# Kernel optimization log

Measured on AMD Instinct MI355X. Metric: run time of the kernel, lower is better.

The kernel has to match this reference:

```python
import jax, jax.numpy as jnp
import numpy as np

N, E = 384, 3072          # nodes, relation pairs
CIN, EMB, D = 4096, 200, 512  # roi feat dim, glove dim, hidden dim
NOBJ, NREL = 151, 51
NUM_ITER = 3
ALPHA = 0.5


def setup_inputs() -> dict:
    key = jax.random.key(0)
    ks = iter(jax.random.split(key, 64))

    def w(shape, scale=0.02):
        return jax.random.normal(next(ks), shape, dtype=jnp.float32) * scale

    inp = {
        'x': jax.random.normal(next(ks), (N, CIN), dtype=jnp.float32),
        'pos_info': jax.random.uniform(next(ks), (N, 9), dtype=jnp.float32),
        'union_features': jax.random.normal(next(ks), (E, CIN), dtype=jnp.float32),
        'obj_labels': jax.random.randint(next(ks), (N,), 0, NOBJ, dtype=jnp.int32),
        'rel_pair_idx': jax.random.randint(next(ks), (E, 2), 0, N, dtype=jnp.int32),
        # embeddings
        'obj_embed1_w': w((NOBJ, EMB)),
        'obj_embed2_w': w((NOBJ, EMB)),
        # node/edge embeddings
        'node_emb_w': w((D, CIN + EMB + 128)), 'node_emb_b': jnp.zeros((D,)),
        'node_emb2_w': w((D, CIN + EMB + D)), 'node_emb2_b': jnp.zeros((D,)),
        'edge_emb_w': w((D, CIN)), 'edge_emb_b': jnp.zeros((D,)),
        # pos_embed: Linear(9,32) -> BN(32) -> Linear(32,128) -> ReLU
        'pos_w1': w((32, 9)), 'pos_b1': jnp.zeros((32,)),
        'pos_gamma': jnp.ones((32,)), 'pos_beta': jnp.zeros((32,)),
        'pos_w2': w((128, 32)), 'pos_b2': jnp.zeros((128,)),
        # node GRUCell (with bias), edge GRUCell (no bias); gate order r,z,n
        'ngate_wih': w((3 * D, D)), 'ngate_whh': w((3 * D, D)),
        'ngate_bih': jnp.zeros((3 * D,)), 'ngate_bhh': jnp.zeros((3 * D,)),
        'egate_wih': w((3 * D, D)), 'egate_whh': w((3 * D, D)),
        # message kernels
        'n2n_w1': w((D, D)), 'n2n_b1': jnp.zeros((D,)),
        'n2n_w2': w((D, D)), 'n2n_b2': jnp.zeros((D,)),
        'e2n_w1': w((D, D)), 'e2n_b1': jnp.zeros((D,)),
        'e2n_w2': w((D, D)), 'e2n_b2': jnp.zeros((D,)),
        # node2edge 1x1 convs == pointwise linears
        'n2e_w1': w((D, 2 * D)), 'n2e_b1': jnp.zeros((D,)),
        'n2e_w2': w((D, D)), 'n2e_b2': jnp.zeros((D,)),
        'rel_cls_w': w((NREL, D)), 'rel_cls_b': jnp.zeros((NREL,)),
    }
    return inp


def _gru(x, h, wih, whh, bih=None, bhh=None):
    gi = x @ wih.T
    gh = h @ whh.T
    if bih is not None:
        gi = gi + bih
        gh = gh + bhh
    ir, iz, ig = jnp.split(gi, 3, axis=-1)
    hr, hz, hg = jnp.split(gh, 3, axis=-1)
    r = jax.nn.sigmoid(ir + hr)
    z = jax.nn.sigmoid(iz + hz)
    g = jnp.tanh(ig + r * hg)
    return (1.0 - z) * g + z * h


def _mlp2(h, w1, b1, w2, b2):
    h = jax.nn.relu(h @ w1.T + b1)
    return jax.nn.relu(h @ w2.T + b2)


def reference(x, pos_info, union_features, obj_labels, rel_pair_idx,
              obj_embed1_w, obj_embed2_w,
              node_emb_w, node_emb_b, node_emb2_w, node_emb2_b,
              edge_emb_w, edge_emb_b,
              pos_w1, pos_b1, pos_gamma, pos_beta, pos_w2, pos_b2,
              ngate_wih, ngate_whh, ngate_bih, ngate_bhh,
              egate_wih, egate_whh,
              n2n_w1, n2n_b1, n2n_w2, n2n_b2,
              e2n_w1, e2n_b1, e2n_w2, e2n_b2,
              n2e_w1, n2e_b1, n2e_w2, n2e_b2,
              rel_cls_w, rel_cls_b):
    n = x.shape[0]
    # pos embed (BatchNorm in training mode = batch stats)
    ph = pos_info @ pos_w1.T + pos_b1
    mu, var = ph.mean(0), ph.var(0)
    ph = (ph - mu) * jax.lax.rsqrt(var + 1e-5) * pos_gamma + pos_beta
    pos_embed = jax.nn.relu(ph @ pos_w2.T + pos_b2)

    obj_embed = obj_embed1_w[obj_labels]  # predcls: GT labels
    node_states = jnp.concatenate([x, obj_embed, pos_embed], -1) @ node_emb_w.T + node_emb_b

    p0, p1 = rel_pair_idx[:, 0], rel_pair_idx[:, 1]
    adj = jnp.zeros((n, n), jnp.float32).at[p0, p1].set(1.0)
    edge_rep = union_features @ edge_emb_w.T + edge_emb_b
    # torch sparse to_dense sums duplicate indices
    edge_states = jnp.zeros((n, n, D), jnp.float32).at[p0, p1].add(edge_rep)

    deg = adj.sum(1, keepdims=True) + 1e-6
    for _ in range(NUM_ITER):
        n2n = (adj @ node_states) / deg
        e2n = jnp.einsum('ij,ijd->jd', adj, edge_states)
        n2n = _mlp2(n2n, n2n_w1, n2n_b1, n2n_w2, n2n_b2)
        e2n = _mlp2(e2n, e2n_w1, e2n_b1, e2n_w2, e2n_b2)
        node_states = _gru(ALPHA * n2n + (1.0 - ALPHA) * e2n, node_states,
                           ngate_wih, ngate_whh, ngate_bih, ngate_bhh)

    # predcls: obj_dists = to_onehot(labels), preds = labels
    obj_dists = jnp.full((n, NOBJ), -1000.0, jnp.float32).at[jnp.arange(n), obj_labels].set(1000.0)
    node_states = jnp.concatenate([x, node_states, obj_embed2_w[obj_labels]], -1) @ node_emb2_w.T + node_emb2_b

    for _ in range(NUM_ITER):
        # all-pairs direction-aware concat, masked by adjacency
        ek = jnp.concatenate([
            jnp.broadcast_to(node_states[:, None, :], (n, n, D)),
            jnp.broadcast_to(node_states[None, :, :], (n, n, D)),
        ], -1) * adj[:, :, None]                      # [n, n, 2D]
        msg = _mlp2(ek, n2e_w1, n2e_b1, n2e_w2, n2e_b2)  # 1x1 convs == pointwise
        edge_states = _gru(msg.reshape(n * n, D), edge_states.reshape(n * n, D),
                           egate_wih, egate_whh).reshape(n, n, D)

    rel_feats = edge_states[p0, p1]
    rel_dists = rel_feats @ rel_cls_w.T + rel_cls_b
    return obj_dists, rel_dists
```

## Files before the change

### kernel.cpp

```cpp
#include <hip/hip_runtime.h>

typedef unsigned short ushort_t;
typedef unsigned int uint_t;

#define N_    384
#define E_    3072
#define CIN_  4096
#define EMB_  200
#define D_    512
#define NOBJ_ 151
#define NREL_ 51
#define K1_   (CIN_ + EMB_ + 128)
#define K1P_  4448
#define K2_   (CIN_ + EMB_ + D_)
#define K2P_  4832

__device__ __forceinline__ ushort_t f2b(float f) {
    uint_t u = __float_as_uint(f);
    u += 0x7FFFu + ((u >> 16) & 1u);
    return (ushort_t)(u >> 16);
}

__global__ void k_pair_min(const int* __restrict__ rp, int* __restrict__ mapMin) {
    int e = blockIdx.x * blockDim.x + threadIdx.x;
    if (e >= E_) return;
    atomicMin(&mapMin[rp[2 * e] * N_ + rp[2 * e + 1]], e);
}
__global__ void k_pair_rep(const int* __restrict__ rp, const int* __restrict__ mapMin,
                           int* __restrict__ rep, int* __restrict__ deg_cnt) {
    int e = blockIdx.x * blockDim.x + threadIdx.x;
    if (e >= E_) return;
    int r = mapMin[rp[2 * e] * N_ + rp[2 * e + 1]];
    rep[e] = r;
    if (r == e) atomicAdd(&deg_cnt[rp[2 * e]], 1);
}
__global__ void k_inv_deg(const int* __restrict__ deg_cnt, float* __restrict__ inv_deg) {
    int i = blockIdx.x * blockDim.x + threadIdx.x;
    if (i < N_) inv_deg[i] = 1.0f / ((float)deg_cnt[i] + 1e-6f);
}

__global__ __launch_bounds__(1024) void k_pos_a(const float* __restrict__ pi,
                                                const float* __restrict__ w1,
                                                const float* __restrict__ b1,
                                                const float* __restrict__ g,
                                                const float* __restrict__ be,
                                                float* __restrict__ posn) {
    __shared__ float ph[N_ * 32];
    __shared__ float mu_s[32], rs_s[32];
    int tid = threadIdx.x;
    for (int idx = tid; idx < N_ * 32; idx += 1024) {
        int i = idx >> 5, f = idx & 31;
        float s = b1[f];
        for (int k = 0; k < 9; ++k) s += pi[i * 9 + k] * w1[f * 9 + k];
        ph[idx] = s;
    }
    __syncthreads();
    if (tid < 32) {
        float s = 0.f;
        for (int i = 0; i < N_; ++i) s += ph[i * 32 + tid];
        float m = s / N_;
        float v = 0.f;
        for (int i = 0; i < N_; ++i) { float d = ph[i * 32 + tid] - m; v += d * d; }
        mu_s[tid] = m;
        rs_s[tid] = rsqrtf(v / N_ + 1e-5f);
    }
    __syncthreads();
    for (int idx = tid; idx < N_ * 32; idx += 1024) {
        int f = idx & 31;
        posn[idx] = (ph[idx] - mu_s[f]) * rs_s[f] * g[f] + be[f];
    }
}
__global__ void k_pos2(const float* __restrict__ pn, const float* __restrict__ w,
                       const float* __restrict__ b, float* __restrict__ out) {
    int idx = blockIdx.x * blockDim.x + threadIdx.x;
    if (idx >= N_ * 128) return;
    int i = idx / 128, f = idx % 128;
    float s = b[f];
    for (int k = 0; k < 32; ++k) s += pn[i * 32 + k] * w[f * 32 + k];
    out[idx] = fmaxf(s, 0.f);
}

__global__ void k_build_A1b(const float* __restrict__ x, const int* __restrict__ lab,
                            const float* __restrict__ emb1, const float* __restrict__ pe,
                            ushort_t* __restrict__ A) {
    int idx = blockIdx.x * blockDim.x + threadIdx.x;
    if (idx >= N_ * K1P_) return;
    int i = idx / K1P_, c = idx % K1P_;
    float v = 0.f;
    if (c < CIN_)             v = x[(size_t)i * CIN_ + c];
    else if (c < CIN_ + EMB_) v = emb1[lab[i] * EMB_ + (c - CIN_)];
    else if (c < K1_)         v = pe[i * 128 + (c - CIN_ - EMB_)];
    A[idx] = f2b(v);
}
__global__ void k_build_A2b(const float* __restrict__ x, const int* __restrict__ lab,
                            const float* __restrict__ emb2, const ushort_t* __restrict__ nsb,
                            ushort_t* __restrict__ A) {
    int idx = blockIdx.x * blockDim.x + threadIdx.x;
    if (idx >= N_ * K2P_) return;
    int i = idx / K2P_, c = idx % K2P_;
    ushort_t o = 0;
    if (c < CIN_)             o = f2b(x[(size_t)i * CIN_ + c]);
    else if (c < CIN_ + D_)   o = nsb[i * D_ + (c - CIN_)];
    else if (c < K2_)         o = f2b(emb2[lab[i] * EMB_ + (c - CIN_ - D_)]);
    A[idx] = o;
}
__global__ void k_build_ekb(const int* __restrict__ rp, const ushort_t* __restrict__ nsb,
                            ushort_t* __restrict__ ek) {
    int idx = blockIdx.x * blockDim.x + threadIdx.x;
    if (idx >= E_ * 2 * D_) return;
    int e = idx / (2 * D_), c = idx % (2 * D_);
    ek[idx] = (c < D_) ? nsb[rp[2 * e] * D_ + c] : nsb[rp[2 * e + 1] * D_ + (c - D_)];
}

struct ConvDesc { const float* src; ushort_t* dst; int K, Kp, rows, rowsp; };
struct ConvArgs { ConvDesc d[16]; };
__global__ void k_conv_batch(ConvArgs a) {
    ConvDesc c = a.d[blockIdx.y];
    for (int row = blockIdx.x; row < c.rowsp; row += gridDim.x) {
        const float* src = c.src + (size_t)row * c.K;
        ushort_t* dst = c.dst + (size_t)row * c.Kp;
        bool inrow = row < c.rows;
        for (int k = threadIdx.x * 4; k < c.Kp; k += blockDim.x * 4) {
            uint2 ov = {0u, 0u};
            if (inrow && k < c.K) {
                float4 v = *(const float4*)(src + k);
                ov.x = (uint_t)f2b(v.x) | ((uint_t)f2b(v.y) << 16);
                ov.y = (uint_t)f2b(v.z) | ((uint_t)f2b(v.w) << 16);
            }
            *(uint2*)(dst + k) = ov;
        }
    }
}
__global__ void k_f2b_n(const float* __restrict__ s, ushort_t* __restrict__ d, int n) {
    int i = blockIdx.x * blockDim.x + threadIdx.x;
    if (i < n) d[i] = f2b(s[i]);
}

__global__ void k_scatter_edge(const float* __restrict__ er, const int* __restrict__ rep,
                               float* __restrict__ es) {
    int e = blockIdx.x;
    int d = blockIdx.y * 256 + threadIdx.x;
    atomicAdd(&es[(size_t)rep[e] * D_ + d], er[(size_t)e * D_ + d]);
}
__global__ void k_broadcast_es(const int* __restrict__ rep, float* __restrict__ es,
                               ushort_t* __restrict__ esb) {
    int idx = blockIdx.x * blockDim.x + threadIdx.x;
    if (idx >= E_ * D_) return;
    int e = idx / D_, d = idx % D_;
    float v = es[(size_t)rep[e] * D_ + d];
    es[idx] = v;
    esb[idx] = f2b(v);
}
__global__ void k_scatter_e2n(const int* __restrict__ rp, const int* __restrict__ rep,
                              const float* __restrict__ es, float* __restrict__ e2n) {
    int e = blockIdx.x;
    if (rep[e] != e) return;
    int d = blockIdx.y * 256 + threadIdx.x;
    atomicAdd(&e2n[rp[2 * e + 1] * D_ + d], es[(size_t)e * D_ + d]);
}
__global__ void k_scatter_n2n(const int* __restrict__ rp, const int* __restrict__ rep,
                              const float* __restrict__ ns, float* __restrict__ n2n) {
    int e = blockIdx.x;
    if (rep[e] != e) return;
    int d = blockIdx.y * 256 + threadIdx.x;
    atomicAdd(&n2n[rp[2 * e] * D_ + d], ns[rp[2 * e + 1] * D_ + d]);
}
__global__ void k_scale_rows_b(const float* __restrict__ a, const float* __restrict__ inv_deg,
                               ushort_t* __restrict__ ob) {
    int idx = blockIdx.x * blockDim.x + threadIdx.x;
    if (idx >= N_ * D_) return;
    ob[idx] = f2b(a[idx] * inv_deg[idx / D_]);
}
__global__ void k_combine_b(const float* __restrict__ araw, const float* __restrict__ b2,
                            const float* __restrict__ e2nm, ushort_t* __restrict__ o) {
    int idx = blockIdx.x * blockDim.x + threadIdx.x;
    if (idx >= N_ * D_) return;
    float a = fmaxf(araw[idx] + b2[idx & (D_ - 1)], 0.f);
    o[idx] = f2b(0.5f * a + 0.5f * e2nm[idx]);
}
__global__ void k_epi(const float* __restrict__ raw, const float* __restrict__ bias,
                      float* __restrict__ fo, ushort_t* __restrict__ bo,
                      int total, int colmask, int relu) {
    int idx = blockIdx.x * blockDim.x + threadIdx.x;
    if (idx >= total) return;
    float v = raw[idx] + bias[idx & colmask];
    if (relu) v = fmaxf(v, 0.f);
    if (fo) fo[idx] = v;
    if (bo) bo[idx] = f2b(v);
}
__global__ void k_epi_rel(const float* __restrict__ raw, const float* __restrict__ relb,
                          float* __restrict__ out) {
    int idx = blockIdx.x * blockDim.x + threadIdx.x;
    if (idx >= E_ * NREL_) return;
    int row = idx / NREL_, col = idx % NREL_;
    out[idx] = raw[row * 64 + col] + relb[col];
}
__global__ void k_gru(const float* __restrict__ gi, const float* __restrict__ gh,
                      const float* __restrict__ bih, const float* __restrict__ bhh,
                      float* __restrict__ h, ushort_t* __restrict__ hb, int M) {
    int idx = blockIdx.x * blockDim.x + threadIdx.x;
    if (idx >= M * D_) return;
    int m = idx / D_, d = idx % D_;
    size_t b3 = (size_t)m * 3 * D_;
    float ir = gi[b3 + d], iz = gi[b3 + D_ + d], ig = gi[b3 + 2 * D_ + d];
    float hr = gh[b3 + d], hz = gh[b3 + D_ + d], hg = gh[b3 + 2 * D_ + d];
    if (bih) { ir += bih[d]; iz += bih[D_ + d]; ig += bih[2 * D_ + d]; }
    if (bhh) { hr += bhh[d]; hz += bhh[D_ + d]; hg += bhh[2 * D_ + d]; }
    float r = 1.f / (1.f + expf(-(ir + hr)));
    float z = 1.f / (1.f + expf(-(iz + hz)));
    float g = tanhf(ig + r * hg);
    size_t hi = (size_t)m * D_ + d;
    float nv = (1.f - z) * g + z * h[hi];
    h[hi] = nv;
    if (hb) hb[hi] = f2b(nv);
}
__global__ void k_obj_dists(const int* __restrict__ lab, float* __restrict__ out) {
    int idx = blockIdx.x * blockDim.x + threadIdx.x;
    if (idx >= N_ * NOBJ_) return;
    out[idx] = (idx % NOBJ_ == lab[idx / NOBJ_]) ? 1000.f : -1000.f;
}

typedef __attribute__((ext_vector_type(8))) short sh8;
typedef __attribute__((ext_vector_type(4))) float f32x4;

#define GLOAD_LDS16(gp, lp)                                                        \
    __builtin_amdgcn_global_load_lds((__attribute__((address_space(1))) void*)(gp),\
                                     (__attribute__((address_space(3))) void*)(lp),\
                                     16, 0, 0)

template <bool SWZ>
__device__ __forceinline__ void get_bxyz(int& bx, int& by, int& bz) {
    if (!SWZ) { bx = blockIdx.x; by = blockIdx.y; bz = blockIdx.z; return; }
    int nx = gridDim.x, nz = gridDim.z;
    int bid = blockIdx.x + nx * (blockIdx.y + gridDim.y * blockIdx.z);
    int r8 = bid & 7, i = bid >> 3;
    int per = nx * nz;
    int ygrp = i / per;
    int rem = i - ygrp * per;
    bx = rem % nx;
    bz = rem / nx;
    by = r8 + 8 * ygrp;
}

template <int FM, int FN>
__device__ __forceinline__ void gemm_kloop(ushort_t* As, ushort_t* Bs,
                                           const ushort_t* __restrict__ A,
                                           const ushort_t* __restrict__ B,
                                           f32x4 (&acc)[FM][FN],
                                           int K, int ks0, int ks1, int bm, int bn) {
    constexpr int BM = FM * 32, BN = FN * 32;
    constexpr int ATILES = (BM + 63) / 64, BTILES = (BN + 63) / 64;
    const int tid = threadIdx.x;
    const int lane = tid & 63, wid = tid >> 6;
    const int wr = wid >> 1, wc = wid & 1;
    const int ar = tid >> 2, ac = (tid & 3) * 8;
    const int l15 = lane & 15, lg = lane >> 4;
    for (int ks = ks0; ks < ks1; ++ks) {
        int k0 = ks * 32;
#pragma unroll
        for (int i = 0; i < ATILES; ++i) {
            int r = i * 64 + ar;
            if ((BM & 63) == 0 || r < BM)
                GLOAD_LDS16(A + (size_t)(bm + r) * K + k0 + ac, &As[r * 32 + ac]);
        }
#pragma unroll
        for (int i = 0; i < BTILES; ++i) {
            int r = i * 64 + ar;
            if ((BN & 63) == 0 || r < BN)
                GLOAD_LDS16(B + (size_t)(bn + r) * K + k0 + ac, &Bs[r * 32 + ac]);
        }
        __syncthreads();
        sh8 af[FM], bf[FN];
#pragma unroll
        for (int m = 0; m < FM; ++m)
            af[m] = *(const sh8*)&As[(wr * FM * 16 + m * 16 + l15) * 32 + lg * 8];
#pragma unroll
        for (int n = 0; n < FN; ++n)
            bf[n] = *(const sh8*)&Bs[(wc * FN * 16 + n * 16 + l15) * 32 + lg * 8];
#pragma unroll
        for (int m = 0; m < FM; ++m)
#pragma unroll
            for (int n = 0; n < FN; ++n)
                acc[m][n] = __builtin_amdgcn_mfma_f32_16x16x32_bf16(af[m], bf[n], acc[m][n], 0, 0, 0);
        __syncthreads();
    }
}

template <int FM, int FN, bool SWZ = false>
__global__ __launch_bounds__(256) void gemm_mfma(const ushort_t* __restrict__ A,
                                                 const ushort_t* __restrict__ B,
                                                 const float* __restrict__ bias,
                                                 float* __restrict__ C,
                                                 ushort_t* __restrict__ Cb,
                                                 int M, int N, int K, int relu) {
    __shared__ ushort_t As[FM * 32 * 32];
    __shared__ ushort_t Bs[FN * 32 * 32];
    int bx, by, bz;
    get_bxyz<SWZ>(bx, by, bz);
    const int bm = by * FM * 32, bn = bx * FN * 32;
    f32x4 acc[FM][FN];
#pragma unroll
    for (int m = 0; m < FM; ++m)
#pragma unroll
        for (int n = 0; n < FN; ++n) acc[m][n] = (f32x4){0.f, 0.f, 0.f, 0.f};
    gemm_kloop<FM, FN>(As, Bs, A, B, acc, K, 0, K / 32, bm, bn);
    const int lane = threadIdx.x & 63, wid = threadIdx.x >> 6;
    const int l15 = lane & 15, lg = lane >> 4;
    const int r0 = bm + (wid >> 1) * FM * 16, c0 = bn + (wid & 1) * FN * 16;
#pragma unroll
    for (int m = 0; m < FM; ++m)
#pragma unroll
        for (int n = 0; n < FN; ++n)
#pragma unroll
            for (int j = 0; j < 4; ++j) {
                int row = r0 + m * 16 + lg * 4 + j;
                int col = c0 + n * 16 + l15;
                if (row < M && col < N) {
                    float v = acc[m][n][j] + (bias ? bias[col] : 0.f);
                    if (relu) v = fmaxf(v, 0.f);
                    if (C)  C[(size_t)row * N + col] = v;
                    if (Cb) Cb[(size_t)row * N + col] = f2b(v);
                }
            }
}

template <int FM, int FN, bool SWZ = false>
__global__ __launch_bounds__(256) void gemm_splitk(const ushort_t* __restrict__ A,
                                                   const ushort_t* __restrict__ B,
                                                   float* __restrict__ C,
                                                   int M, int N, int K, int S) {
    __shared__ ushort_t As[FM * 32 * 32];
    __shared__ ushort_t Bs[FN * 32 * 32];
    int bx, by, bz;
    get_bxyz<SWZ>(bx, by, bz);
    const int nsteps = K / 32;
    const int ss = (nsteps + S - 1) / S;
    const int ks0 = bz * ss;
    const int ks1 = min(nsteps, ks0 + ss);
    if (ks0 >= ks1) return;
    const int bm = by * FM * 32, bn = bx * FN * 32;
    f32x4 acc[FM][FN];
#pragma unroll
    for (int m = 0; m < FM; ++m)
#pragma unroll
        for (int n = 0; n < FN; ++n) acc[m][n] = (f32x4){0.f, 0.f, 0.f, 0.f};
    gemm_kloop<FM, FN>(As, Bs, A, B, acc, K, ks0, ks1, bm, bn);
    const int lane = threadIdx.x & 63, wid = threadIdx.x >> 6;
    const int l15 = lane & 15, lg = lane >> 4;
    const int r0 = bm + (wid >> 1) * FM * 16, c0 = bn + (wid & 1) * FN * 16;
#pragma unroll
    for (int m = 0; m < FM; ++m)
#pragma unroll
        for (int n = 0; n < FN; ++n)
#pragma unroll
            for (int j = 0; j < 4; ++j) {
                int row = r0 + m * 16 + lg * 4 + j;
                int col = c0 + n * 16 + l15;
                if (row < M && col < N)
                    atomicAdd(&C[(size_t)row * N + col], acc[m][n][j]);
            }
}

__global__ __launch_bounds__(256) void k_ghe_gru(const ushort_t* __restrict__ esb_in,
                                                 const ushort_t* __restrict__ W,
                                                 const float* __restrict__ gi,
                                                 const float* __restrict__ es_in,
                                                 float* __restrict__ es_out,
                                                 ushort_t* __restrict__ esb_out) {
    __shared__ ushort_t As[64 * 32];
    __shared__ ushort_t Bs[96 * 32];
    int bid = blockIdx.x + gridDim.x * blockIdx.y;
    int r8 = bid & 7, i = bid >> 3;
    int per = gridDim.x;
    int ygrp = i / per;
    int x = i - ygrp * per;
    int y = r8 + 8 * ygrp;
    const int bm = y * 64;
    const int dcol0 = x * 32;
    const int tid = threadIdx.x;
    const int lane = tid & 63, wid = tid >> 6;
    const int wr = wid >> 1, wc = wid & 1;
    const int ar = tid >> 2, ac = (tid & 3) * 8;
    const int l15 = lane & 15, lg = lane >> 4;
    f32x4 acc[2][3];
#pragma unroll
    for (int m = 0; m < 2; ++m)
#pragma unroll
        for (int g = 0; g < 3; ++g) acc[m][g] = (f32x4){0.f, 0.f, 0.f, 0.f};

    for (int k0 = 0; k0 < D_; k0 += 32) {
        GLOAD_LDS16(esb_in + (size_t)(bm + ar) * D_ + k0 + ac, &As[ar * 32 + ac]);
        {
            int rr = ar;
            int wrow = (rr >> 5) * D_ + dcol0 + (rr & 31);
            GLOAD_LDS16(W + (size_t)wrow * D_ + k0 + ac, &Bs[rr * 32 + ac]);
        }
        if (tid < 128) {
            int rr = 64 + ar;
            int wrow = 2 * D_ + dcol0 + (rr & 31);
            GLOAD_LDS16(W + (size_t)wrow * D_ + k0 + ac, &Bs[rr * 32 + ac]);
        }
        __syncthreads();
        sh8 af[2], bf[3];
#pragma unroll
        for (int m = 0; m < 2; ++m)
            af[m] = *(const sh8*)&As[(wr * 32 + m * 16 + l15) * 32 + lg * 8];
#pragma unroll
        for (int g = 0; g < 3; ++g)
            bf[g] = *(const sh8*)&Bs[(g * 32 + wc * 16 + l15) * 32 + lg * 8];
#pragma unroll
        for (int m = 0; m < 2; ++m)
#pragma unroll
            for (int g = 0; g < 3; ++g)
                acc[m][g] = __builtin_amdgcn_mfma_f32_16x16x32_bf16(af[m], bf[g], acc[m][g], 0, 0, 0);
        __syncthreads();
    }

    const int d = dcol0 + wc * 16 + l15;
#pragma unroll
    for (int m = 0; m < 2; ++m)
#pragma unroll
        for (int j = 0; j < 4; ++j) {
            int row = bm + wr * 32 + m * 16 + lg * 4 + j;
            size_t gbase = (size_t)row * 1536 + d;
            float r = 1.f / (1.f + expf(-(gi[gbase] + acc[m][0][j])));
            float z = 1.f / (1.f + expf(-(gi[gbase + 512] + acc[m][1][j])));
            float g = tanhf(gi[gbase + 1024] + r * acc[m][2][j]);
            float hv = es_in[(size_t)row * D_ + d];
            float nv = (1.f - z) * g + z * hv;
            es_out[(size_t)row * D_ + d] = nv;
            esb_out[(size_t)row * D_ + d] = f2b(nv);
        }
}

static inline dim3 mgrid(int M, int N, int FM, int FN) {
    return dim3((N + FN * 32 - 1) / (FN * 32), (M + FM * 32 - 1) / (FM * 32));
}
static inline dim3 sgrid(int M, int N, int FM, int FN, int S) {
    dim3 g = mgrid(M, N, FM, FN);
    return dim3(g.x, g.y, S);
}

extern "C" void kernel_launch(void* const* d_in, const int* in_sizes, int n_in,
                              void* d_out, int out_size, void* d_ws, size_t ws_size,
                              hipStream_t stream) {
    const float* x      = (const float*)d_in[0];
    const float* posi   = (const float*)d_in[1];
    const float* unionf = (const float*)d_in[2];
    const int*   lab    = (const int*)d_in[3];
    const int*   rp     = (const int*)d_in[4];
    const float* emb1   = (const float*)d_in[5];
    const float* emb2   = (const float*)d_in[6];
    const float* nw     = (const float*)d_in[7];
    const float* nb     = (const float*)d_in[8];
    const float* nw2    = (const float*)d_in[9];
    const float* nb2    = (const float*)d_in[10];
    const float* ew     = (const float*)d_in[11];
    const float* eb     = (const float*)d_in[12];
    const float* pw1    = (const float*)d_in[13];
    const float* pb1    = (const float*)d_in[14];
    const float* pg     = (const float*)d_in[15];
    const float* pbe    = (const float*)d_in[16];
    const float* pw2    = (const float*)d_in[17];
    const float* pb2    = (const float*)d_in[18];
    const float* ngwih  = (const float*)d_in[19];
    const float* ngwhh  = (const float*)d_in[20];
    const float* ngbih  = (const float*)d_in[21];
    const float* ngbhh  = (const float*)d_in[22];
    const float* egwih  = (const float*)d_in[23];
    const float* egwhh  = (const float*)d_in[24];
    const float* n2nw1  = (const float*)d_in[25];
    const float* n2nb1  = (const float*)d_in[26];
    const float* n2nw2  = (const float*)d_in[27];
    const float* n2nb2  = (const float*)d_in[28];
    const float* e2nw1  = (const float*)d_in[29];
    const float* e2nb1  = (const float*)d_in[30];
    const float* e2nw2  = (const float*)d_in[31];
    const float* e2nb2  = (const float*)d_in[32];
    const float* n2ew1  = (const float*)d_in[33];
    const float* n2eb1  = (const float*)d_in[34];
    const float* n2ew2  = (const float*)d_in[35];
    const float* n2eb2  = (const float*)d_in[36];
    const float* relw   = (const float*)d_in[37];
    const float* relb   = (const float*)d_in[38];

    size_t off = 0;
    auto alloc = [&](size_t bytes) {
        off = (off + 255) & ~(size_t)255;
        char* p = (char*)d_ws + off;
        off += bytes;
        return (void*)p;
    };
    int*      mapMin  = (int*)alloc((size_t)N_ * N_ * 4);
    int*      rep     = (int*)alloc(E_ * 4);
    int*      deg_cnt = (int*)alloc(N_ * 4);
    float*    inv_deg = (float*)alloc(N_ * 4);
    float*    posn    = (float*)alloc(N_ * 32 * 4);
    float*    pe      = (float*)alloc(N_ * 128 * 4);
    float*    ns      = (float*)alloc((size_t)N_ * D_ * 4);
    ushort_t* nsb     = (ushort_t*)alloc((size_t)N_ * D_ * 2);
    float*    nsraw   = (float*)alloc((size_t)N_ * D_ * 4);
    char*     scrR    = (char*)alloc((size_t)(3 * N_ * D_ + 2 * N_ * 3 * D_) * 4);
    float*    n2n     = (float*)scrR;
    float*    tmpraw  = (float*)(scrR + (size_t)N_ * D_ * 4);
    float*    n2nmraw = (float*)(scrR + (size_t)2 * N_ * D_ * 4);
    float*    gin     = (float*)(scrR + (size_t)3 * N_ * D_ * 4);
    float*    ghn     = (float*)(scrR + (size_t)(3 * N_ * D_ + N_ * 3 * D_) * 4);
    const size_t scrBytes = (size_t)(3 * N_ * D_ + 2 * N_ * 3 * D_) * 4;
    float*    e2nm    = (float*)alloc((size_t)N_ * D_ * 4);
    float*    relraw  = (float*)alloc((size_t)E_ * 64 * 4);
    char*     unionU  = (char*)alloc((size_t)E_ * 2 * D_ * 2);
    ushort_t* A1b = (ushort_t*)unionU;
    ushort_t* A2b = (ushort_t*)unionU;
    ushort_t* ekb = (ushort_t*)unionU;
    char*     ufbU = (char*)alloc((size_t)E_ * CIN_ * 2);
    ushort_t* ufb = (ushort_t*)ufbU;
    float*    gie = (float*)ufbU;
    char*     erepU = (char*)alloc((size_t)E_ * D_ * 4);
    float*    erep  = (float*)erepU;
    ushort_t* erepb = (ushort_t*)erepU;
    ushort_t* msgb  = (ushort_t*)(erepU + (size_t)E_ * D_ * 2);
    float*    es    = (float*)alloc((size_t)E_ * D_ * 4);
    ushort_t* esb   = (ushort_t*)alloc((size_t)E_ * D_ * 2);
    float*    es2   = (float*)alloc((size_t)E_ * D_ * 4);
    ushort_t* esb2  = (ushort_t*)alloc((size_t)E_ * D_ * 2);
    float*    e2n   = (float*)alloc((size_t)N_ * D_ * 4);
    ushort_t* e2nb  = (ushort_t*)alloc((size_t)N_ * D_ * 2);
    ushort_t* tmpb  = (ushort_t*)alloc((size_t)N_ * D_ * 2);
    ushort_t* n2nb  = (ushort_t*)alloc((size_t)N_ * D_ * 2);
    ushort_t* xinb  = (ushort_t*)alloc((size_t)N_ * D_ * 2);
    ushort_t* nwb     = (ushort_t*)alloc((size_t)D_ * K1P_ * 2);
    ushort_t* nw2b    = (ushort_t*)alloc((size_t)D_ * K2P_ * 2);
    ushort_t* ewb     = (ushort_t*)alloc((size_t)D_ * CIN_ * 2);
    ushort_t* ngwihb  = (ushort_t*)alloc((size_t)3 * D_ * D_ * 2);
    ushort_t* ngwhhb  = (ushort_t*)alloc((size_t)3 * D_ * D_ * 2);
    ushort_t* egwihb  = (ushort_t*)alloc((size_t)3 * D_ * D_ * 2);
    ushort_t* egwhhb  = (ushort_t*)alloc((size_t)3 * D_ * D_ * 2);
    ushort_t* n2nw1b  = (ushort_t*)alloc((size_t)D_ * D_ * 2);
    ushort_t* n2nw2b  = (ushort_t*)alloc((size_t)D_ * D_ * 2);
    ushort_t* e2nw1b  = (ushort_t*)alloc((size_t)D_ * D_ * 2);
    ushort_t* e2nw2b  = (ushort_t*)alloc((size_t)D_ * D_ * 2);
    ushort_t* n2ew1b  = (ushort_t*)alloc((size_t)D_ * 2 * D_ * 2);
    ushort_t* n2ew2b  = (ushort_t*)alloc((size_t)D_ * D_ * 2);
    ushort_t* relwb   = (ushort_t*)alloc((size_t)64 * D_ * 2);
    if (off > ws_size) return;

    float* out_obj = (float*)d_out;
    float* out_rel = (float*)d_out + N_ * NOBJ_;

    ConvArgs ca;
    int ci = 0;
    auto addc = [&](const float* s, ushort_t* dptr, int K, int Kp, int rows, int rowsp) {
        ca.d[ci++] = ConvDesc{s, dptr, K, Kp, rows, rowsp};
    };
    addc(nw,    nwb,    K1_,      K1P_,     D_,       D_);
    addc(nw2,   nw2b,   K2_,      K2P_,     D_,       D_);
    addc(ew,    ewb,    CIN_,     CIN_,     D_,       D_);
    addc(ngwih, ngwihb, D_,       D_,       3 * D_,   3 * D_);
    addc(ngwhh, ngwhhb, D_,       D_,       3 * D_,   3 * D_);
    addc(egwih, egwihb, D_,       D_,       3 * D_,   3 * D_);
    addc(egwhh, egwhhb, D_,       D_,       3 * D_,   3 * D_);
    addc(n2nw1, n2nw1b, D_,       D_,       D_,       D_);
    addc(n2nw2, n2nw2b, D_,       D_,       D_,       D_);
    addc(e2nw1, e2nw1b, D_,       D_,       D_,       D_);
    addc(e2nw2, e2nw2b, D_,       D_,       D_,       D_);
    addc(n2ew1, n2ew1b, 2 * D_,   2 * D_,   D_,       D_);
    addc(n2ew2, n2ew2b, D_,       D_,       D_,       D_);
    addc(relw,  relwb,  D_,       D_,       NREL_,    64);
    addc(unionf, ufb,   CIN_,     CIN_,     E_,       E_);
    for (; ci < 16;) ca.d[ci++] = ConvDesc{nullptr, nullptr, 4, 4, 0, 0};
    k_conv_batch<<<dim3(512, 15), 256, 0, stream>>>(ca);

    (void)hipMemsetAsync(mapMin, 0x7F, (size_t)N_ * N_ * 4, stream);
    (void)hipMemsetAsync(deg_cnt, 0, N_ * 4, stream);
    k_pair_min<<<(E_ + 255) / 256, 256, 0, stream>>>(rp, mapMin);
    k_pair_rep<<<(E_ + 255) / 256, 256, 0, stream>>>(rp, mapMin, rep, deg_cnt);
    k_inv_deg<<<(N_ + 255) / 256, 256, 0, stream>>>(deg_cnt, inv_deg);

    k_pos_a<<<1, 1024, 0, stream>>>(posi, pw1, pb1, pg, pbe, posn);
    k_pos2<<<(N_ * 128 + 255) / 256, 256, 0, stream>>>(posn, pw2, pb2, pe);

    k_build_A1b<<<((size_t)N_ * K1P_ + 255) / 256, 256, 0, stream>>>(x, lab, emb1, pe, A1b);
    (void)hipMemsetAsync(nsraw, 0, (size_t)N_ * D_ * 4, stream);
    gemm_splitk<1, 1><<<sgrid(N_, D_, 1, 1, 8), 256, 0, stream>>>(A1b, nwb, nsraw, N_, D_, K1P_, 8);
    k_epi<<<(N_ * D_ + 255) / 256, 256, 0, stream>>>(nsraw, nb, ns, nsb, N_ * D_, D_ - 1, 0);

    (void)hipMemsetAsync(erep, 0, (size_t)E_ * D_ * 4, stream);
    gemm_splitk<2, 2, true><<<sgrid(E_, D_, 2, 2, 4), 256, 0, stream>>>(ufb, ewb, erep, E_, D_, CIN_, 4);
    k_epi<<<((size_t)E_ * D_ + 255) / 256, 256, 0, stream>>>(erep, eb, erep, nullptr, E_ * D_, D_ - 1, 0);
    (void)hipMemsetAsync(es, 0, (size_t)E_ * D_ * 4, stream);
    k_scatter_edge<<<dim3(E_, 2), 256, 0, stream>>>(erep, rep, es);
    k_broadcast_es<<<(E_ * D_ + 255) / 256, 256, 0, stream>>>(rep, es, esb);

    (void)hipMemsetAsync(e2n, 0, (size_t)N_ * D_ * 4, stream);
    k_scatter_e2n<<<dim3(E_, 2), 256, 0, stream>>>(rp, rep, es, e2n);
    k_f2b_n<<<(N_ * D_ + 255) / 256, 256, 0, stream>>>(e2n, e2nb, N_ * D_);
    (void)hipMemsetAsync(scrR, 0, scrBytes, stream);
    gemm_splitk<1, 1><<<sgrid(N_, D_, 1, 1, 8), 256, 0, stream>>>(e2nb, e2nw1b, tmpraw, N_, D_, D_, 8);
    k_epi<<<(N_ * D_ + 255) / 256, 256, 0, stream>>>(tmpraw, e2nb1, nullptr, tmpb, N_ * D_, D_ - 1, 1);
    gemm_splitk<1, 1><<<sgrid(N_, D_, 1, 1, 8), 256, 0, stream>>>(tmpb, e2nw2b, n2nmraw, N_, D_, D_, 8);
    k_epi<<<(N_ * D_ + 255) / 256, 256, 0, stream>>>(n2nmraw, e2nb2, e2nm, nullptr, N_ * D_, D_ - 1, 1);

    for (int it = 0; it < 3; ++it) {
        (void)hipMemsetAsync(scrR, 0, scrBytes, stream);
        k_scatter_n2n<<<dim3(E_, 2), 256, 0, stream>>>(rp, rep, ns, n2n);
        k_scale_rows_b<<<(N_ * D_ + 255) / 256, 256, 0, stream>>>(n2n, inv_deg, n2nb);
        gemm_splitk<1, 1><<<sgrid(N_, D_, 1, 1, 8), 256, 0, stream>>>(n2nb, n2nw1b, tmpraw, N_, D_, D_, 8);
        k_epi<<<(N_ * D_ + 255) / 256, 256, 0, stream>>>(tmpraw, n2nb1, nullptr, tmpb, N_ * D_, D_ - 1, 1);
        gemm_splitk<1, 1><<<sgrid(N_, D_, 1, 1, 8), 256, 0, stream>>>(tmpb, n2nw2b, n2nmraw, N_, D_, D_, 8);
        k_combine_b<<<(N_ * D_ + 255) / 256, 256, 0, stream>>>(n2nmraw, n2nb2, e2nm, xinb);
        gemm_splitk<1, 1><<<sgrid(N_, 3 * D_, 1, 1, 4), 256, 0, stream>>>(xinb, ngwihb, gin, N_, 3 * D_, D_, 4);
        gemm_splitk<1, 1><<<sgrid(N_, 3 * D_, 1, 1, 4), 256, 0, stream>>>(nsb, ngwhhb, ghn, N_, 3 * D_, D_, 4);
        k_gru<<<(N_ * D_ + 255) / 256, 256, 0, stream>>>(gin, ghn, ngbih, ngbhh, ns, nsb, N_);
    }

    k_obj_dists<<<(N_ * NOBJ_ + 255) / 256, 256, 0, stream>>>(lab, out_obj);

    k_build_A2b<<<((size_t)N_ * K2P_ + 255) / 256, 256, 0, stream>>>(x, lab, emb2, nsb, A2b);
    (void)hipMemsetAsync(nsraw, 0, (size_t)N_ * D_ * 4, stream);
    gemm_splitk<1, 1><<<sgrid(N_, D_, 1, 1, 8), 256, 0, stream>>>(A2b, nw2b, nsraw, N_, D_, K2P_, 8);
    k_epi<<<(N_ * D_ + 255) / 256, 256, 0, stream>>>(nsraw, nb2, ns, nsb, N_ * D_, D_ - 1, 0);

    k_build_ekb<<<((size_t)E_ * 2 * D_ + 255) / 256, 256, 0, stream>>>(rp, nsb, ekb);
    gemm_mfma<2, 2, true><<<mgrid(E_, D_, 2, 2), 256, 0, stream>>>(ekb, n2ew1b, n2eb1, nullptr, erepb, E_, D_, 2 * D_, 1);
    gemm_mfma<2, 2, true><<<mgrid(E_, D_, 2, 2), 256, 0, stream>>>(erepb, n2ew2b, n2eb2, nullptr, msgb, E_, D_, D_, 1);
    gemm_mfma<2, 4, true><<<mgrid(E_, 3 * D_, 2, 4), 256, 0, stream>>>(msgb, egwihb, nullptr, gie, nullptr, E_, 3 * D_, D_, 0);
    {
        float* esI = es;  ushort_t* esbI = esb;
        float* esO = es2; ushort_t* esbO = esb2;
        for (int it = 0; it < 3; ++it) {
            k_ghe_gru<<<dim3(16, 48), 256, 0, stream>>>(esbI, egwhhb, gie, esI, esO, esbO);
            float* tf = esI; esI = esO; esO = tf;
            ushort_t* tb = esbI; esbI = esbO; esbO = tb;
        }
        (void)hipMemsetAsync(relraw, 0, (size_t)E_ * 64 * 4, stream);
        gemm_splitk<1, 1><<<sgrid(E_, 64, 1, 1, 4), 256, 0, stream>>>(esbI, relwb, relraw, E_, 64, D_, 4);
        k_epi_rel<<<(E_ * NREL_ + 255) / 256, 256, 0, stream>>>(relraw, relb, out_rel);
    }
}
```

Before: 664.4 us.

## Fuse node message-passing loop into one cooperative persistent kernel

Replaces the node-side sequence of scatter, conversion, split-K GEMM, epilogue and GRU launches with a single cooperative kernel that runs every stage in turn, separated by grid-wide syncs, and fuses the epilogues into the GEMM stores without split-K. It also moves the union-feature conversion out of the batched conversion kernel into a dedicated vectorized kernel. The aim is to remove the overhead of dozens of small launches and memsets. In exchange it relies on grid.sync latency and a fixed 256-block grid, which may underuse the GPU for the larger GEMMs.

```diff
diff --git a/kernel.cpp b/kernel.cpp
--- a/kernel.cpp
+++ b/kernel.cpp
@@ -1,4 +1,7 @@
 #include <hip/hip_runtime.h>
+#include <hip/hip_cooperative_groups.h>
+
+namespace cg = cooperative_groups;
 
 typedef unsigned short ushort_t;
 typedef unsigned int uint_t;
@@ -112,8 +115,17 @@
     ek[idx] = (c < D_) ? nsb[rp[2 * e] * D_ + c] : nsb[rp[2 * e + 1] * D_ + (c - D_)];
 }
 
+__global__ void k_conv_uf(const float* __restrict__ src, ushort_t* __restrict__ dst) {
+    int i = blockIdx.x * blockDim.x + threadIdx.x;
+    if (i >= E_ * CIN_ / 4) return;
+    float4 v = ((const float4*)src)[i];
+    uint2 o;
+    o.x = (uint_t)f2b(v.x) | ((uint_t)f2b(v.y) << 16);
+    o.y = (uint_t)f2b(v.z) | ((uint_t)f2b(v.w) << 16);
+    ((uint2*)dst)[i] = o;
+}
 struct ConvDesc { const float* src; ushort_t* dst; int K, Kp, rows, rowsp; };
-struct ConvArgs { ConvDesc d[16]; };
+struct ConvArgs { ConvDesc d[14]; };
 __global__ void k_conv_batch(ConvArgs a) {
     ConvDesc c = a.d[blockIdx.y];
     for (int row = blockIdx.x; row < c.rowsp; row += gridDim.x) {
@@ -131,10 +143,6 @@
         }
     }
 }
-__global__ void k_f2b_n(const float* __restrict__ s, ushort_t* __restrict__ d, int n) {
-    int i = blockIdx.x * blockDim.x + threadIdx.x;
-    if (i < n) d[i] = f2b(s[i]);
-}
 
 __global__ void k_scatter_edge(const float* __restrict__ er, const int* __restrict__ rep,
                                float* __restrict__ es) {
@@ -150,33 +158,6 @@
     float v = es[(size_t)rep[e] * D_ + d];
     es[idx] = v;
     esb[idx] = f2b(v);
-}
-__global__ void k_scatter_e2n(const int* __restrict__ rp, const int* __restrict__ rep,
-                              const float* __restrict__ es, float* __restrict__ e2n) {
-    int e = blockIdx.x;
-    if (rep[e] != e) return;
-    int d = blockIdx.y * 256 + threadIdx.x;
-    atomicAdd(&e2n[rp[2 * e + 1] * D_ + d], es[(size_t)e * D_ + d]);
-}
-__global__ void k_scatter_n2n(const int* __restrict__ rp, const int* __restrict__ rep,
-                              const float* __restrict__ ns, float* __restrict__ n2n) {
-    int e = blockIdx.x;
-    if (rep[e] != e) return;
-    int d = blockIdx.y * 256 + threadIdx.x;
-    atomicAdd(&n2n[rp[2 * e] * D_ + d], ns[rp[2 * e + 1] * D_ + d]);
-}
-__global__ void k_scale_rows_b(const float* __restrict__ a, const float* __restrict__ inv_deg,
-                               ushort_t* __restrict__ ob) {
-    int idx = blockIdx.x * blockDim.x + threadIdx.x;
-    if (idx >= N_ * D_) return;
-    ob[idx] = f2b(a[idx] * inv_deg[idx / D_]);
-}
-__global__ void k_combine_b(const float* __restrict__ araw, const float* __restrict__ b2,
-                            const float* __restrict__ e2nm, ushort_t* __restrict__ o) {
-    int idx = blockIdx.x * blockDim.x + threadIdx.x;
-    if (idx >= N_ * D_) return;
-    float a = fmaxf(araw[idx] + b2[idx & (D_ - 1)], 0.f);
-    o[idx] = f2b(0.5f * a + 0.5f * e2nm[idx]);
 }
 __global__ void k_epi(const float* __restrict__ raw, const float* __restrict__ bias,
                       float* __restrict__ fo, ushort_t* __restrict__ bo,
@@ -194,25 +175,6 @@
     if (idx >= E_ * NREL_) return;
     int row = idx / NREL_, col = idx % NREL_;
     out[idx] = raw[row * 64 + col] + relb[col];
-}
-__global__ void k_gru(const float* __restrict__ gi, const float* __restrict__ gh,
-                      const float* __restrict__ bih, const float* __restrict__ bhh,
-                      float* __restrict__ h, ushort_t* __restrict__ hb, int M) {
-    int idx = blockIdx.x * blockDim.x + threadIdx.x;
-    if (idx >= M * D_) return;
-    int m = idx / D_, d = idx % D_;
-    size_t b3 = (size_t)m * 3 * D_;
-    float ir = gi[b3 + d], iz = gi[b3 + D_ + d], ig = gi[b3 + 2 * D_ + d];
-    float hr = gh[b3 + d], hz = gh[b3 + D_ + d], hg = gh[b3 + 2 * D_ + d];
-    if (bih) { ir += bih[d]; iz += bih[D_ + d]; ig += bih[2 * D_ + d]; }
-    if (bhh) { hr += bhh[d]; hz += bhh[D_ + d]; hg += bhh[2 * D_ + d]; }
-    float r = 1.f / (1.f + expf(-(ir + hr)));
-    float z = 1.f / (1.f + expf(-(iz + hz)));
-    float g = tanhf(ig + r * hg);
-    size_t hi = (size_t)m * D_ + d;
-    float nv = (1.f - z) * g + z * h[hi];
-    h[hi] = nv;
-    if (hb) hb[hi] = f2b(nv);
 }
 __global__ void k_obj_dists(const int* __restrict__ lab, float* __restrict__ out) {
     int idx = blockIdx.x * blockDim.x + threadIdx.x;
@@ -431,6 +393,117 @@
             es_out[(size_t)row * D_ + d] = nv;
             esb_out[(size_t)row * D_ + d] = f2b(nv);
         }
+}
+
+struct NodeArgs {
+    const int* rp; const int* rep; const float* inv_deg;
+    const float* es;
+    float* e2n; ushort_t* e2nb; float* e2nm;
+    const ushort_t* e2nw1b; const float* e2nb1;
+    const ushort_t* e2nw2b; const float* e2nb2;
+    const ushort_t* n2nw1b; const float* n2nb1;
+    const ushort_t* n2nw2b; const float* n2nb2;
+    const ushort_t* ngwihb; const ushort_t* ngwhhb;
+    const float* ngbih; const float* ngbhh;
+    float* n2n; ushort_t* n2nbuf; ushort_t* tmpb; ushort_t* xinb;
+    float* gin; float* ghn;
+    float* ns; ushort_t* nsb;
+};
+
+template <int FN, int MODE>
+__device__ __forceinline__ void coop_gemm(ushort_t* As, ushort_t* Bs,
+                                          const ushort_t* __restrict__ A,
+                                          const ushort_t* __restrict__ B,
+                                          int Nn,
+                                          const float* __restrict__ bias,
+                                          const float* __restrict__ aux,
+                                          float* __restrict__ fo,
+                                          ushort_t* __restrict__ bo) {
+    const int tN = Nn / (FN * 32);
+    const int ntiles = (N_ / 32) * tN;
+    const int lane = threadIdx.x & 63, wid = threadIdx.x >> 6;
+    const int l15 = lane & 15, lg = lane >> 4;
+    for (int t = blockIdx.x; t < ntiles; t += gridDim.x) {
+        int by = t / tN, bx = t - by * tN;
+        int bm = by * 32, bn = bx * FN * 32;
+        f32x4 acc[1][FN];
+#pragma unroll
+        for (int n = 0; n < FN; ++n) acc[0][n] = (f32x4){0.f, 0.f, 0.f, 0.f};
+        gemm_kloop<1, FN>(As, Bs, A, B, acc, D_, 0, D_ / 32, bm, bn);
+        const int r0 = bm + (wid >> 1) * 16, c0 = bn + (wid & 1) * FN * 16;
+#pragma unroll
+        for (int n = 0; n < FN; ++n)
+#pragma unroll
+            for (int j = 0; j < 4; ++j) {
+                int row = r0 + lg * 4 + j;
+                int col = c0 + n * 16 + l15;
+                size_t idx = (size_t)row * Nn + col;
+                float v = acc[0][n][j];
+                if (MODE == 0) { v = fmaxf(v + bias[col], 0.f); bo[idx] = f2b(v); }
+                if (MODE == 1) { v = fmaxf(v + bias[col], 0.f); fo[idx] = v; }
+                if (MODE == 2) { v = fmaxf(v + bias[col], 0.f); bo[idx] = f2b(0.5f * v + 0.5f * aux[idx]); }
+                if (MODE == 3) { fo[idx] = v; }
+            }
+    }
+}
+
+__global__ __launch_bounds__(256) void k_node_all(NodeArgs a) {
+    cg::grid_group grid = cg::this_grid();
+    __shared__ ushort_t As[32 * 32];
+    __shared__ ushort_t Bs[256 * 32];
+    const int gsz = gridDim.x * blockDim.x;
+    const int gid = blockIdx.x * blockDim.x + threadIdx.x;
+
+    for (int i = gid; i < N_ * D_; i += gsz) { a.e2n[i] = 0.f; a.n2n[i] = 0.f; }
+    grid.sync();
+    for (int i = gid; i < E_ * D_; i += gsz) {
+        int e = i >> 9, d = i & 511;
+        if (a.rep[e] == e) atomicAdd(&a.e2n[a.rp[2 * e + 1] * D_ + d], a.es[(size_t)e * D_ + d]);
+    }
+    grid.sync();
+    for (int i = gid; i < N_ * D_; i += gsz) a.e2nb[i] = f2b(a.e2n[i]);
+    grid.sync();
+    coop_gemm<2, 0>(As, Bs, a.e2nb, a.e2nw1b, D_, a.e2nb1, nullptr, nullptr, a.tmpb);
+    grid.sync();
+    coop_gemm<2, 1>(As, Bs, a.tmpb, a.e2nw2b, D_, a.e2nb2, nullptr, a.e2nm, nullptr);
+    grid.sync();
+
+    for (int it = 0; it < 3; ++it) {
+        for (int i = gid; i < E_ * D_; i += gsz) {
+            int e = i >> 9, d = i & 511;
+            if (a.rep[e] == e) atomicAdd(&a.n2n[a.rp[2 * e] * D_ + d], a.ns[a.rp[2 * e + 1] * D_ + d]);
+        }
+        grid.sync();
+        for (int i = gid; i < N_ * D_; i += gsz) {
+            a.n2nbuf[i] = f2b(a.n2n[i] * a.inv_deg[i >> 9]);
+            a.n2n[i] = 0.f;
+        }
+        grid.sync();
+        coop_gemm<2, 0>(As, Bs, a.n2nbuf, a.n2nw1b, D_, a.n2nb1, nullptr, nullptr, a.tmpb);
+        grid.sync();
+        coop_gemm<2, 2>(As, Bs, a.tmpb, a.n2nw2b, D_, a.n2nb2, a.e2nm, nullptr, a.xinb);
+        grid.sync();
+        coop_gemm<8, 3>(As, Bs, a.xinb, a.ngwihb, 3 * D_, nullptr, nullptr, a.gin, nullptr);
+        coop_gemm<8, 3>(As, Bs, a.nsb, a.ngwhhb, 3 * D_, nullptr, nullptr, a.ghn, nullptr);
+        grid.sync();
+        for (int i = gid; i < N_ * D_; i += gsz) {
+            int d = i & 511;
+            size_t b3 = (size_t)(i >> 9) * 1536;
+            float ir = a.gin[b3 + d] + a.ngbih[d];
+            float iz = a.gin[b3 + 512 + d] + a.ngbih[512 + d];
+            float ig = a.gin[b3 + 1024 + d] + a.ngbih[1024 + d];
+            float hr = a.ghn[b3 + d] + a.ngbhh[d];
+            float hz = a.ghn[b3 + 512 + d] + a.ngbhh[512 + d];
+            float hg = a.ghn[b3 + 1024 + d] + a.ngbhh[1024 + d];
+            float r = 1.f / (1.f + expf(-(ir + hr)));
+            float z = 1.f / (1.f + expf(-(iz + hz)));
+            float g = tanhf(ig + r * hg);
+            float nv = (1.f - z) * g + z * a.ns[i];
+            a.ns[i] = nv;
+            a.nsb[i] = f2b(nv);
+        }
+        grid.sync();
+    }
 }
 
 static inline dim3 mgrid(int M, int N, int FM, int FN) {
@@ -500,13 +573,9 @@
     float*    ns      = (float*)alloc((size_t)N_ * D_ * 4);
     ushort_t* nsb     = (ushort_t*)alloc((size_t)N_ * D_ * 2);
     float*    nsraw   = (float*)alloc((size_t)N_ * D_ * 4);
-    char*     scrR    = (char*)alloc((size_t)(3 * N_ * D_ + 2 * N_ * 3 * D_) * 4);
-    float*    n2n     = (float*)scrR;
-    float*    tmpraw  = (float*)(scrR + (size_t)N_ * D_ * 4);
-    float*    n2nmraw = (float*)(scrR + (size_t)2 * N_ * D_ * 4);
-    float*    gin     = (float*)(scrR + (size_t)3 * N_ * D_ * 4);
-    float*    ghn     = (float*)(scrR + (size_t)(3 * N_ * D_ + N_ * 3 * D_) * 4);
-    const size_t scrBytes = (size_t)(3 * N_ * D_ + 2 * N_ * 3 * D_) * 4;
+    float*    n2n     = (float*)alloc((size_t)N_ * D_ * 4);
+    float*    gin     = (float*)alloc((size_t)N_ * 3 * D_ * 4);
+    float*    ghn     = (float*)alloc((size_t)N_ * 3 * D_ * 4);
     float*    e2nm    = (float*)alloc((size_t)N_ * D_ * 4);
     float*    relraw  = (float*)alloc((size_t)E_ * 64 * 4);
     char*     unionU  = (char*)alloc((size_t)E_ * 2 * D_ * 2);
@@ -548,6 +617,7 @@
     float* out_obj = (float*)d_out;
     float* out_rel = (float*)d_out + N_ * NOBJ_;
 
+    k_conv_uf<<<(E_ * CIN_ / 4 + 255) / 256, 256, 0, stream>>>(unionf, ufb);
     ConvArgs ca;
     int ci = 0;
     auto addc = [&](const float* s, ushort_t* dptr, int K, int Kp, int rows, int rowsp) {
@@ -567,9 +637,7 @@
     addc(n2ew1, n2ew1b, 2 * D_,   2 * D_,   D_,       D_);
     addc(n2ew2, n2ew2b, D_,       D_,       D_,       D_);
     addc(relw,  relwb,  D_,       D_,       NREL_,    64);
-    addc(unionf, ufb,   CIN_,     CIN_,     E_,       E_);
-    for (; ci < 16;) ca.d[ci++] = ConvDesc{nullptr, nullptr, 4, 4, 0, 0};
-    k_conv_batch<<<dim3(512, 15), 256, 0, stream>>>(ca);
+    k_conv_batch<<<dim3(512, 14), 256, 0, stream>>>(ca);
 
     (void)hipMemsetAsync(mapMin, 0x7F, (size_t)N_ * N_ * 4, stream);
     (void)hipMemsetAsync(deg_cnt, 0, N_ * 4, stream);
@@ -592,26 +660,22 @@
     k_scatter_edge<<<dim3(E_, 2), 256, 0, stream>>>(erep, rep, es);
     k_broadcast_es<<<(E_ * D_ + 255) / 256, 256, 0, stream>>>(rep, es, esb);
 
-    (void)hipMemsetAsync(e2n, 0, (size_t)N_ * D_ * 4, stream);
-    k_scatter_e2n<<<dim3(E_, 2), 256, 0, stream>>>(rp, rep, es, e2n);
-    k_f2b_n<<<(N_ * D_ + 255) / 256, 256, 0, stream>>>(e2n, e2nb, N_ * D_);
-    (void)hipMemsetAsync(scrR, 0, scrBytes, stream);
-    gemm_splitk<1, 1><<<sgrid(N_, D_, 1, 1, 8), 256, 0, stream>>>(e2nb, e2nw1b, tmpraw, N_, D_, D_, 8);
-    k_epi<<<(N_ * D_ + 255) / 256, 256, 0, stream>>>(tmpraw, e2nb1, nullptr, tmpb, N_ * D_, D_ - 1, 1);
-    gemm_splitk<1, 1><<<sgrid(N_, D_, 1, 1, 8), 256, 0, stream>>>(tmpb, e2nw2b, n2nmraw, N_, D_, D_, 8);
-    k_epi<<<(N_ * D_ + 255) / 256, 256, 0, stream>>>(n2nmraw, e2nb2, e2nm, nullptr, N_ * D_, D_ - 1, 1);
-
-    for (int it = 0; it < 3; ++it) {
-        (void)hipMemsetAsync(scrR, 0, scrBytes, stream);
-        k_scatter_n2n<<<dim3(E_, 2), 256, 0, stream>>>(rp, rep, ns, n2n);
-        k_scale_rows_b<<<(N_ * D_ + 255) / 256, 256, 0, stream>>>(n2n, inv_deg, n2nb);
-        gemm_splitk<1, 1><<<sgrid(N_, D_, 1, 1, 8), 256, 0, stream>>>(n2nb, n2nw1b, tmpraw, N_, D_, D_, 8);
-        k_epi<<<(N_ * D_ + 255) / 256, 256, 0, stream>>>(tmpraw, n2nb1, nullptr, tmpb, N_ * D_, D_ - 1, 1);
-        gemm_splitk<1, 1><<<sgrid(N_, D_, 1, 1, 8), 256, 0, stream>>>(tmpb, n2nw2b, n2nmraw, N_, D_, D_, 8);
-        k_combine_b<<<(N_ * D_ + 255) / 256, 256, 0, stream>>>(n2nmraw, n2nb2, e2nm, xinb);
-        gemm_splitk<1, 1><<<sgrid(N_, 3 * D_, 1, 1, 4), 256, 0, stream>>>(xinb, ngwihb, gin, N_, 3 * D_, D_, 4);
-        gemm_splitk<1, 1><<<sgrid(N_, 3 * D_, 1, 1, 4), 256, 0, stream>>>(nsb, ngwhhb, ghn, N_, 3 * D_, D_, 4);
-        k_gru<<<(N_ * D_ + 255) / 256, 256, 0, stream>>>(gin, ghn, ngbih, ngbhh, ns, nsb, N_);
+    {
+        NodeArgs na;
+        na.rp = rp; na.rep = rep; na.inv_deg = inv_deg; na.es = es;
+        na.e2n = e2n; na.e2nb = e2nb; na.e2nm = e2nm;
+        na.e2nw1b = e2nw1b; na.e2nb1 = e2nb1;
+        na.e2nw2b = e2nw2b; na.e2nb2 = e2nb2;
+        na.n2nw1b = n2nw1b; na.n2nb1 = n2nb1;
+        na.n2nw2b = n2nw2b; na.n2nb2 = n2nb2;
+        na.ngwihb = ngwihb; na.ngwhhb = ngwhhb;
+        na.ngbih = ngbih; na.ngbhh = ngbhh;
+        na.n2n = n2n; na.n2nbuf = n2nb; na.tmpb = tmpb; na.xinb = xinb;
+        na.gin = gin; na.ghn = ghn;
+        na.ns = ns; na.nsb = nsb;
+        void* kargs[] = { &na };
+        (void)hipLaunchCooperativeKernel((const void*)k_node_all, dim3(256), dim3(256),
+                                         kargs, 0, stream);
     }
 
     k_obj_dists<<<(N_ * NOBJ_ + 255) / 256, 256, 0, stream>>>(lab, out_obj);
```

Result: slower. 1.329 ms (+100.1%).
